# Performance work log

Measured on AMD Instinct MI355X. Metric: run time of the kernel, lower is better.

The kernel has to match this reference:

```python
import jax, jax.numpy as jnp
import numpy as np


def setup_inputs() -> dict:
    key = jax.random.key(0)
    k1, k2, k3 = jax.random.split(key, 3)
    num, c_in, c_out, nx, ny, din, dout = 128, 3, 8, 31, 31, 4, 6
    x = jax.random.normal(k1, (num, c_in, din, nx + 1, ny + 1), dtype=jnp.float32)
    tensors = jax.random.normal(k2, (c_in, c_out, nx, ny, din, din, din, din, dout), dtype=jnp.float32)
    bias = jax.random.normal(k3, (c_out, nx, ny, dout), dtype=jnp.float32) * 1e-8
    return {"x": x, "tensors": tensors, "bias": bias}


def reference(x, tensors, bias):
    # x: [num, c_in, din, sx, sy]; tensors: [c_in, c_out, nx, ny, din,din,din,din, dout]
    num, c_in, din, sx, sy = x.shape
    X, Y = sx - 1, sy - 1  # == nx, ny
    c_out, dout = tensors.shape[1], tensors.shape[-1]
    # four 2x2-patch corners, each [num, c_in, din, X, Y]
    a = x[:, :, :, :-1, :-1]
    b = x[:, :, :, 1:, :-1]
    c = x[:, :, :, :-1, 1:]
    d = x[:, :, :, 1:, 1:]
    # outer product of the four corner vectors -> rank-4 local feature [num, c_in, din^4, X, Y]
    ab = jnp.einsum('ncixy,ncjxy->ncijxy', a, b)
    cd = jnp.einsum('nckxy,nclxy->ncklxy', c, d)
    patch = jnp.einsum('ncijxy,ncklxy->ncijklxy', ab, cd)
    patch = patch.reshape(num, c_in, din ** 4, X, Y)
    # per-position weight: [c_in, c_out, X, Y, din^4, dout]
    w = tensors.reshape(c_in, c_out, X, Y, din ** 4, dout)
    out = jnp.einsum('ncmxy,cpxymo->npoxy', patch, w)  # [num, c_out, dout, X, Y]
    out = out + bias.transpose(0, 3, 1, 2)[None]  # bias -> [1, c_out, dout, X, Y]
    return out
```

## Files before the change

### kernel.cpp

```cpp
#include <hip/hip_runtime.h>


typedef __attribute__((ext_vector_type(8))) short short8;
typedef __attribute__((ext_vector_type(4))) float floatx4;
typedef __attribute__((ext_vector_type(4))) unsigned int uintx4;

#define WS_ELEMS (961u * 6144u)
#define SA_STR 72
#define SW_STR 72

static __device__ __forceinline__ unsigned short f2bf(float f) {
  union { float f; unsigned u; } v; v.f = f;
  unsigned r = v.u + 0x7FFFu + ((v.u >> 16) & 1u);
  return (unsigned short)(r >> 16);
}

template <bool TO_WS>
__global__ __launch_bounds__(256, 4)
void ttn_conv_mfma(const float* __restrict__ x,
                   const float* __restrict__ tensors,
                   const float* __restrict__ bias,
                   float* __restrict__ dst) {
  __shared__ __align__(16) unsigned short sA[128 * SA_STR];
  __shared__ __align__(16) unsigned short sW[48 * SW_STR];

  const int site = blockIdx.x;
  const int xx = site / 31, yy = site - xx * 31;
  const int t = threadIdx.x;
  const int lane = t & 63, wave = t >> 6;
  const int row = lane & 15, quad = lane >> 4;

  const int n_st = t & 127;
  const int h = t >> 7;
  const int p_st = t >> 5;
  const int q_st = t & 31;

  floatx4 acc[2][3];
#pragma unroll
  for (int i0 = 0; i0 < 2; ++i0)
#pragma unroll
    for (int j0 = 0; j0 < 3; ++j0)
      acc[i0][j0] = (floatx4){0.f, 0.f, 0.f, 0.f};

  float areg[4], b0 = 0.f, b1 = 0.f, cdreg[16];
  float4 wv0, wv1, wv2;

  {
    const float* src = tensors + ((size_t)(p_st * 961 + site)) * 1536 + 12 * q_st;
    wv0 = *(const float4*)src;
    wv1 = *(const float4*)(src + 4);
    wv2 = *(const float4*)(src + 8);
  }

#pragma unroll
  for (int ch = 0; ch < 12; ++ch) {
    const int mb = ch & 3;
    if ((ch & 3) == 0) {
      const int c = ch >> 2;
      const float* xp = x + ((size_t)n_st * 3 + c) * 4096 + xx * 32 + yy;
      float bq[4], cq[4], dq[4];
#pragma unroll
      for (int i = 0; i < 4; ++i) {
        const float* r0 = xp + i * 1024;
        areg[i] = r0[0];
        cq[i]   = r0[1];
        bq[i]   = r0[32];
        dq[i]   = r0[33];
      }
      b0 = h ? bq[2] : bq[0];
      b1 = h ? bq[3] : bq[1];
#pragma unroll
      for (int k2 = 0; k2 < 4; ++k2)
#pragma unroll
        for (int l2 = 0; l2 < 4; ++l2)
          cdreg[k2 * 4 + l2] = cq[k2] * dq[l2];
    }
    __syncthreads();

    {
      const float vv[12] = {wv0.x, wv0.y, wv0.z, wv0.w, wv1.x, wv1.y,
                            wv1.z, wv1.w, wv2.x, wv2.y, wv2.z, wv2.w};
#pragma unroll
      for (int o = 0; o < 6; ++o) {
        const unsigned pk = (unsigned)f2bf(vv[o]) | ((unsigned)f2bf(vv[o + 6]) << 16);
        *(unsigned*)&sW[(p_st * 6 + o) * SW_STR + 2 * q_st] = pk;
      }
    }
#pragma unroll
    for (int e = 0; e < 2; ++e) {
      const float ab = areg[mb] * (e ? b1 : b0);
      unsigned pk[8];
#pragma unroll
      for (int u = 0; u < 8; ++u)
        pk[u] = (unsigned)f2bf(ab * cdreg[2 * u]) |
                ((unsigned)f2bf(ab * cdreg[2 * u + 1]) << 16);
      uintx4* dp = (uintx4*)&sA[n_st * SA_STR + (2 * h + e) * 16];
      uintx4 v0 = {pk[0], pk[1], pk[2], pk[3]};
      uintx4 v1 = {pk[4], pk[5], pk[6], pk[7]};
      dp[0] = v0;
      dp[1] = v1;
    }
    if (ch < 11) {
      const int cn = (ch + 1) >> 2, mbn = (ch + 1) & 3;
      const float* src = tensors +
          ((size_t)((cn * 8 + p_st) * 961 + site)) * 1536 + (mbn * 64 + 2 * q_st) * 6;
      wv0 = *(const float4*)src;
      wv1 = *(const float4*)(src + 4);
      wv2 = *(const float4*)(src + 8);
    }
    __syncthreads();

#pragma unroll
    for (int ks = 0; ks < 2; ++ks) {
      const int kof = ks * 32 + quad * 8;
      short8 af[2], bf[3];
#pragma unroll
      for (int mt = 0; mt < 2; ++mt)
        af[mt] = *(const short8*)&sA[(wave * 32 + mt * 16 + row) * SA_STR + kof];
#pragma unroll
      for (int nt = 0; nt < 3; ++nt)
        bf[nt] = *(const short8*)&sW[(nt * 16 + row) * SW_STR + kof];
#pragma unroll
      for (int mt = 0; mt < 2; ++mt)
#pragma unroll
        for (int nt = 0; nt < 3; ++nt)
          acc[mt][nt] = __builtin_amdgcn_mfma_f32_16x16x32_bf16(
              af[mt], bf[nt], acc[mt][nt], 0, 0, 0);
    }
  }

  if (TO_WS) {
#pragma unroll
    for (int mt = 0; mt < 2; ++mt)
#pragma unroll
      for (int r = 0; r < 4; ++r) {
        const int n = wave * 32 + mt * 16 + quad * 4 + r;
#pragma unroll
        for (int nt = 0; nt < 3; ++nt) {
          const int po = nt * 16 + row;
          dst[(size_t)site * 6144 + n * 48 + po] = acc[mt][nt][r];
        }
      }
  } else {
#pragma unroll
    for (int mt = 0; mt < 2; ++mt)
#pragma unroll
      for (int r = 0; r < 4; ++r) {
        const int n = wave * 32 + mt * 16 + quad * 4 + r;
#pragma unroll
        for (int nt = 0; nt < 3; ++nt) {
          const int po = nt * 16 + row;
          const int p = po / 6, o = po - p * 6;
          dst[(size_t)(n * 48 + po) * 961 + site] =
              acc[mt][nt][r] + bias[(p * 961 + site) * 6 + o];
        }
      }
  }
}

__global__ __launch_bounds__(256, 8)
void ttn_transpose_bias(const float* __restrict__ ws,
                        const float* __restrict__ bias,
                        float* __restrict__ out) {
  __shared__ float tile[32][33];
  const int f0 = blockIdx.x * 32;
  const int s0 = blockIdx.y * 32;
  const int tx = threadIdx.x;
  const int ty = threadIdx.y;

#pragma unroll
  for (int rr = 0; rr < 4; ++rr) {
    const int srow = ty + rr * 8;
    const int site = s0 + srow;
    if (site < 961)
      tile[srow][tx] = ws[(size_t)site * 6144 + f0 + tx];
  }
  __syncthreads();

#pragma unroll
  for (int rr = 0; rr < 4; ++rr) {
    const int fy = ty + rr * 8;
    const int f = f0 + fy;
    const int site = s0 + tx;
    if (site < 961) {
      const int po = f % 48;
      const int p = po / 6, o = po - p * 6;
      out[(size_t)f * 961 + site] = tile[tx][fy] + bias[(p * 961 + site) * 6 + o];
    }
  }
}

extern "C" void kernel_launch(void* const* d_in, const int* in_sizes, int n_in,
                              void* d_out, int out_size, void* d_ws, size_t ws_size,
                              hipStream_t stream) {
  const float* x       = (const float*)d_in[0];
  const float* tensors = (const float*)d_in[1];
  const float* bias    = (const float*)d_in[2];
  float* out           = (float*)d_out;

  const size_t need = (size_t)WS_ELEMS * sizeof(float);
  if (d_ws != nullptr && ws_size >= need) {
    float* ws = (float*)d_ws;
    hipLaunchKernelGGL((ttn_conv_mfma<true>), dim3(961), dim3(256), 0, stream,
                       x, tensors, bias, ws);
    hipLaunchKernelGGL(ttn_transpose_bias, dim3(192, 31), dim3(32, 8), 0, stream,
                       ws, bias, out);
  } else {
    hipLaunchKernelGGL((ttn_conv_mfma<false>), dim3(961), dim3(256), 0, stream,
                       x, tensors, bias, out);
  }
}
```

Measured before the change: 244.2 us.

## Build patch MFMA operands in registers and double-buffer weight tiles in LDS

The rank-4 patch A-operand is no longer staged through shared memory. Each lane now computes its own bf16 fragment directly in registers from per-row corner values. Weight tiles are double-buffered in LDS with a two-deep register prefetch, which cuts the per-chunk barriers from two to one, and the scalar bf16 rounding is swapped for the hardware packed convert instruction. The cost is some redundant x loads and products per lane, plus a possible rounding difference from the hardware conversion.

```diff
diff --git a/kernel.cpp b/kernel.cpp
--- a/kernel.cpp
+++ b/kernel.cpp
@@ -3,16 +3,20 @@
 
 typedef __attribute__((ext_vector_type(8))) short short8;
 typedef __attribute__((ext_vector_type(4))) float floatx4;
-typedef __attribute__((ext_vector_type(4))) unsigned int uintx4;
 
 #define WS_ELEMS (961u * 6144u)
-#define SA_STR 72
 #define SW_STR 72
-
-static __device__ __forceinline__ unsigned short f2bf(float f) {
-  union { float f; unsigned u; } v; v.f = f;
-  unsigned r = v.u + 0x7FFFu + ((v.u >> 16) & 1u);
-  return (unsigned short)(r >> 16);
+#define C_STRIDE 11808768
+
+static __device__ __forceinline__ unsigned cvt_pk_bf16(float lo, float hi) {
+  unsigned r;
+  asm("v_cvt_pk_bf16_f32 %0, %1, %2" : "=v"(r) : "v"(lo), "v"(hi));
+  return r;
+}
+
+static __device__ __forceinline__ void barrier_lgkm() {
+  asm volatile("s_waitcnt lgkmcnt(0)\n\ts_barrier" ::: "memory");
+  __builtin_amdgcn_sched_barrier(0);
 }
 
 template <bool TO_WS>
@@ -21,19 +25,16 @@
                    const float* __restrict__ tensors,
                    const float* __restrict__ bias,
                    float* __restrict__ dst) {
-  __shared__ __align__(16) unsigned short sA[128 * SA_STR];
-  __shared__ __align__(16) unsigned short sW[48 * SW_STR];
+  __shared__ __align__(16) unsigned short sW[2][48 * SW_STR];
 
   const int site = blockIdx.x;
   const int xx = site / 31, yy = site - xx * 31;
   const int t = threadIdx.x;
   const int lane = t & 63, wave = t >> 6;
   const int row = lane & 15, quad = lane >> 4;
-
-  const int n_st = t & 127;
-  const int h = t >> 7;
   const int p_st = t >> 5;
   const int q_st = t & 31;
+  const int k0 = (quad & 1) * 2;
 
   floatx4 acc[2][3];
 #pragma unroll
@@ -42,84 +43,92 @@
     for (int j0 = 0; j0 < 3; ++j0)
       acc[i0][j0] = (floatx4){0.f, 0.f, 0.f, 0.f};
 
-  float areg[4], b0 = 0.f, b1 = 0.f, cdreg[16];
-  float4 wv0, wv1, wv2;
-
-  {
-    const float* src = tensors + ((size_t)(p_st * 961 + site)) * 1536 + 12 * q_st;
-    wv0 = *(const float4*)src;
-    wv1 = *(const float4*)(src + 4);
-    wv2 = *(const float4*)(src + 8);
-  }
+  float a_[2][4];
+  float bsel[2][2];
+  float cd_[2][8];
+
+  const float* wbase = tensors + ((size_t)(p_st * 961 + site)) * 1536 + 12 * q_st;
+
+  float4 wa0, wa1, wa2, wb0, wb1, wb2;
+  wa0 = *(const float4*)(wbase + 0);
+  wa1 = *(const float4*)(wbase + 4);
+  wa2 = *(const float4*)(wbase + 8);
+  wb0 = *(const float4*)(wbase + 384);
+  wb1 = *(const float4*)(wbase + 388);
+  wb2 = *(const float4*)(wbase + 392);
 
 #pragma unroll
   for (int ch = 0; ch < 12; ++ch) {
     const int mb = ch & 3;
-    if ((ch & 3) == 0) {
+
+    if (mb == 0) {
       const int c = ch >> 2;
-      const float* xp = x + ((size_t)n_st * 3 + c) * 4096 + xx * 32 + yy;
-      float bq[4], cq[4], dq[4];
-#pragma unroll
-      for (int i = 0; i < 4; ++i) {
-        const float* r0 = xp + i * 1024;
-        areg[i] = r0[0];
-        cq[i]   = r0[1];
-        bq[i]   = r0[32];
-        dq[i]   = r0[33];
-      }
-      b0 = h ? bq[2] : bq[0];
-      b1 = h ? bq[3] : bq[1];
-#pragma unroll
-      for (int k2 = 0; k2 < 4; ++k2)
-#pragma unroll
-        for (int l2 = 0; l2 < 4; ++l2)
-          cdreg[k2 * 4 + l2] = cq[k2] * dq[l2];
-    }
-    __syncthreads();
+#pragma unroll
+      for (int nn = 0; nn < 2; ++nn) {
+        const int n = wave * 32 + nn * 16 + row;
+        const float* xp = x + ((size_t)n * 3 + c) * 4096 + xx * 32 + yy;
+        float bq[4], dq[4];
+#pragma unroll
+        for (int i = 0; i < 4; ++i) {
+          const float* r0 = xp + i * 1024;
+          a_[nn][i] = r0[0];
+          bq[i]     = r0[32];
+          dq[i]     = r0[33];
+        }
+        bsel[nn][0] = (quad & 2) ? bq[1] : bq[0];
+        bsel[nn][1] = (quad & 2) ? bq[3] : bq[2];
+        const float cq0 = xp[k0 * 1024 + 1];
+        const float cq1 = xp[(k0 + 1) * 1024 + 1];
+#pragma unroll
+        for (int l = 0; l < 4; ++l) {
+          cd_[nn][l]     = cq0 * dq[l];
+          cd_[nn][4 + l] = cq1 * dq[l];
+        }
+      }
+    }
 
     {
-      const float vv[12] = {wv0.x, wv0.y, wv0.z, wv0.w, wv1.x, wv1.y,
-                            wv1.z, wv1.w, wv2.x, wv2.y, wv2.z, wv2.w};
-#pragma unroll
-      for (int o = 0; o < 6; ++o) {
-        const unsigned pk = (unsigned)f2bf(vv[o]) | ((unsigned)f2bf(vv[o + 6]) << 16);
-        *(unsigned*)&sW[(p_st * 6 + o) * SW_STR + 2 * q_st] = pk;
-      }
-    }
-#pragma unroll
-    for (int e = 0; e < 2; ++e) {
-      const float ab = areg[mb] * (e ? b1 : b0);
-      unsigned pk[8];
-#pragma unroll
-      for (int u = 0; u < 8; ++u)
-        pk[u] = (unsigned)f2bf(ab * cdreg[2 * u]) |
-                ((unsigned)f2bf(ab * cdreg[2 * u + 1]) << 16);
-      uintx4* dp = (uintx4*)&sA[n_st * SA_STR + (2 * h + e) * 16];
-      uintx4 v0 = {pk[0], pk[1], pk[2], pk[3]};
-      uintx4 v1 = {pk[4], pk[5], pk[6], pk[7]};
-      dp[0] = v0;
-      dp[1] = v1;
-    }
-    if (ch < 11) {
-      const int cn = (ch + 1) >> 2, mbn = (ch + 1) & 3;
-      const float* src = tensors +
-          ((size_t)((cn * 8 + p_st) * 961 + site)) * 1536 + (mbn * 64 + 2 * q_st) * 6;
-      wv0 = *(const float4*)src;
-      wv1 = *(const float4*)(src + 4);
-      wv2 = *(const float4*)(src + 8);
-    }
-    __syncthreads();
+      const float4 w0 = (ch & 1) ? wb0 : wa0;
+      const float4 w1 = (ch & 1) ? wb1 : wa1;
+      const float4 w2 = (ch & 1) ? wb2 : wa2;
+      const float vv[12] = {w0.x, w0.y, w0.z, w0.w, w1.x, w1.y,
+                            w1.z, w1.w, w2.x, w2.y, w2.z, w2.w};
+      unsigned short* dW = &sW[ch & 1][0];
+#pragma unroll
+      for (int o = 0; o < 6; ++o)
+        *(unsigned*)&dW[(p_st * 6 + o) * SW_STR + 2 * q_st] =
+            cvt_pk_bf16(vv[o], vv[o + 6]);
+    }
+
+    if (ch + 2 < 12) {
+      const float* src =
+          wbase + (size_t)((ch + 2) >> 2) * C_STRIDE + ((ch + 2) & 3) * 384;
+      const float4 n0 = *(const float4*)src;
+      const float4 n1 = *(const float4*)(src + 4);
+      const float4 n2 = *(const float4*)(src + 8);
+      if (ch & 1) { wb0 = n0; wb1 = n1; wb2 = n2; }
+      else        { wa0 = n0; wa1 = n1; wa2 = n2; }
+    }
+
+    barrier_lgkm();
 
 #pragma unroll
     for (int ks = 0; ks < 2; ++ks) {
+      short8 af[2], bf[3];
+#pragma unroll
+      for (int mt = 0; mt < 2; ++mt) {
+        const float ab = a_[mt][mb] * bsel[mt][ks];
+        union { unsigned u[4]; short8 s; } pk;
+        pk.u[0] = cvt_pk_bf16(ab * cd_[mt][0], ab * cd_[mt][1]);
+        pk.u[1] = cvt_pk_bf16(ab * cd_[mt][2], ab * cd_[mt][3]);
+        pk.u[2] = cvt_pk_bf16(ab * cd_[mt][4], ab * cd_[mt][5]);
+        pk.u[3] = cvt_pk_bf16(ab * cd_[mt][6], ab * cd_[mt][7]);
+        af[mt] = pk.s;
+      }
       const int kof = ks * 32 + quad * 8;
-      short8 af[2], bf[3];
-#pragma unroll
-      for (int mt = 0; mt < 2; ++mt)
-        af[mt] = *(const short8*)&sA[(wave * 32 + mt * 16 + row) * SA_STR + kof];
 #pragma unroll
       for (int nt = 0; nt < 3; ++nt)
-        bf[nt] = *(const short8*)&sW[(nt * 16 + row) * SW_STR + kof];
+        bf[nt] = *(const short8*)&sW[ch & 1][(nt * 16 + row) * SW_STR + kof];
 #pragma unroll
       for (int mt = 0; mt < 2; ++mt)
 #pragma unroll
```

New measurement: 302.7 us. 1.24x slower.
